# Optimization experiments

Measured on AMD Instinct MI355X. Metric: run time of the kernel, lower is better.

Reference implementation:

```python
import jax, jax.numpy as jnp
import numpy as np

B, L, E, H = 4, 1024, 1024, 16
D = E // H  # head_dim = 64
K = 3       # conv kernel size
PROB = 0.9  # Bernoulli keep probability


def setup_inputs() -> dict:
    key = jax.random.key(0)
    ks = jax.random.split(key, 8)
    query = jax.random.normal(ks[0], (B, L, E), dtype=jnp.float32)
    keys = jax.random.normal(ks[1], (B, L, E), dtype=jnp.float32)
    values = jax.random.normal(ks[2], (B, L, E), dtype=jnp.float32)
    padding_mask = jax.random.randint(ks[3], (B, L), 0, 2, dtype=jnp.int32)
    causal_mask = jax.random.randint(ks[4], (B, L), 0, 2, dtype=jnp.int32)
    bern_mask = jax.random.bernoulli(ks[5], PROB, (B, H, L)).astype(jnp.int32)
    # learned params: grouped conv (one in/out channel per head) and value linear
    conv_w = jax.random.normal(ks[6], (H, 1, K, K), dtype=jnp.float32) * 0.1
    conv_b = jnp.zeros((H,), dtype=jnp.float32)
    Wv = jax.random.normal(ks[7], (D, D), dtype=jnp.float32) / np.sqrt(D)
    return {"query": query, "keys": keys, "values": values,
            "padding_mask": padding_mask, "causal_mask": causal_mask,
            "bern_mask": bern_mask, "conv_w": conv_w, "conv_b": conv_b, "Wv": Wv}


def _split_heads(x):  # [b, l, (h d)] -> [b, h, l, d]
    b, l, _ = x.shape
    return x.reshape(b, l, H, D).transpose(0, 2, 1, 3)


def reference(query, keys, values, padding_mask, causal_mask, bern_mask, conv_w, conv_b, Wv):
    # queries: grouped conv2d over [b, h=channels, l, d], shape-preserving
    q = _split_heads(query)
    q = jax.lax.conv_general_dilated(
        q, conv_w, window_strides=(1, 1), padding=((1, 1), (1, 1)),
        dimension_numbers=("NCHW", "OIHW", "NCHW"), feature_group_count=H)
    q = q + conv_b[None, :, None, None]
    # keys: Bernoulli-masked fill with -inf, softmax over the SEQ dim (dim=-2)
    k = _split_heads(keys)
    k = jnp.where(bern_mask[..., None].astype(bool), k, -jnp.inf)
    k = jax.nn.softmax(k, axis=-2)
    # values: per-head linear (torch Linear: x @ W^T)
    v = jnp.einsum("bhld,ed->bhle", _split_heads(values), Wv)
    # attention
    energy = jnp.einsum("bhqd,bhkd->bhqk", q, k)
    mask = (padding_mask.astype(bool) & causal_mask.astype(bool))  # [b, k]
    energy = jnp.where(mask[:, None, None, :], jnp.float32(-1e20), energy)
    attn = jax.nn.softmax(energy / jnp.sqrt(jnp.float32(E)), axis=-1)
    out = jnp.einsum("bhqk,bhkd->bhqd", attn, v)
    return out.transpose(0, 2, 1, 3).reshape(query.shape[0], query.shape[1], E)
```

## Files before the change

### kernel.cpp

```cpp
#include <hip/hip_runtime.h>
#include <hip/hip_bf16.h>
#include <math.h>

#define BB 4
#define LL 1024
#define EE 1024
#define HH 16
#define DD 64
#define NCH 8
#define CHROWS 128
#define K2C 0.04508422002777998f
#define BIASC 7.2134752044448f

typedef __attribute__((ext_vector_type(8))) short short8;
typedef __attribute__((ext_vector_type(4))) float f32x4;
typedef __attribute__((ext_vector_type(4))) int int4v;

static __device__ __forceinline__ unsigned short bfbits(float x) {
    __hip_bfloat16 h = __float2bfloat16(x);
    return *(unsigned short*)&h;
}

#define CVTPK(dst, lo_, hi_) \
    asm("v_cvt_pk_bf16_f32 %0, %1, %2" : "=v"(dst) : "v"(lo_), "v"(hi_))

__global__ __launch_bounds__(256) void prep_kernel(
    const float* __restrict__ query,
    const float* __restrict__ conv_w,
    const float* __restrict__ conv_b,
    const float* __restrict__ values,
    const float* __restrict__ Wv,
    const float* __restrict__ keys,
    const int* __restrict__ bern,
    const int* __restrict__ pad,
    const int* __restrict__ cau,
    __hip_bfloat16* __restrict__ qcb,
    __hip_bfloat16* __restrict__ vt,
    float* __restrict__ pmax,
    float* __restrict__ psum,
    float* __restrict__ mbias) {
    __shared__ __align__(16) char SM[34048];
    int tid = threadIdx.x;
    int bid = blockIdx.x;

    if (bid < 4096) {
        int d = tid & 63;
        int lr = tid >> 6;
        int l0 = (bid & (LL / 4 - 1)) << 2;
        int bh = bid >> 8;
        int h = bh & (HH - 1);
        int b = bh >> 4;
        int l = l0 + lr;

        const float* w = conv_w + h * 9;
        float acc = conv_b[h];
        const float* qin = query + ((size_t)b * LL) * EE + h * DD;
        #pragma unroll
        for (int i = 0; i < 3; ++i) {
            int li = l + i - 1;
            if (li < 0 || li >= LL) continue;
            #pragma unroll
            for (int j = 0; j < 3; ++j) {
                int dj = d + j - 1;
                if (dj < 0 || dj >= DD) continue;
                acc += w[i * 3 + j] * qin[(size_t)li * EE + dj];
            }
        }
        qcb[((size_t)bh * LL + l) * DD + d] = __float2bfloat16(acc);
    } else if (bid < 5120) {
        float (*WvS)[65] = (float(*)[65])SM;
        float (*vs)[68]  = (float(*)[68])(SM + 16640);
        int tile = bid - 4096;
        int lt = tile & 15;
        int bh = tile >> 4;
        int h = bh & (HH - 1);
        int b = bh >> 4;
        int l0 = lt * 64;

        for (int idx = tid; idx < 64 * 64; idx += 256)
            WvS[idx >> 6][idx & 63] = Wv[idx];
        const float* vin = values + ((size_t)b * LL + l0) * EE + h * DD;
        for (int idx = tid; idx < 1024; idx += 256) {
            int r = idx >> 4;
            int c4 = (idx & 15) << 2;
            *(float4*)&vs[r][c4] = *(const float4*)&vin[(size_t)r * EE + c4];
        }
        __syncthreads();

        int d = tid & 63;
        int r0 = (tid >> 6) * 16;
        float acc[16];
        #pragma unroll
        for (int r = 0; r < 16; ++r) acc[r] = 0.f;
        for (int k = 0; k < 64; ++k) {
            float wv = WvS[d][k];
            #pragma unroll
            for (int r = 0; r < 16; ++r) acc[r] += vs[r0 + r][k] * wv;
        }
        union { unsigned short us[16]; uint2 u2[4]; } pk;
        #pragma unroll
        for (int r = 0; r < 16; ++r) pk.us[r] = bfbits(acc[r]);
        int C32 = (r0 >> 5) << 5;
        int h4 = (r0 >> 4) & 1;
        __hip_bfloat16* vo = vt + ((size_t)bh * DD + d) * LL + l0 + C32 + 4 * h4;
        #pragma unroll
        for (int g2 = 0; g2 < 4; ++g2)
            *(uint2*)&vo[8 * g2] = pk.u2[g2];
    } else {
        float (*sm)[64] = (float(*)[64])SM;
        float (*ss)[64] = (float(*)[64])(SM + 1024);
        int blk = bid - 5120;
        int d = tid & 63;
        int seg = tid >> 6;
        int ch = blk & (NCH - 1);
        int bh = blk >> 3;
        int h = bh & (HH - 1);
        int b = bh >> 4;
        int r0 = ch * CHROWS + seg * 32;

        if (h == 0 && tid < CHROWS) {
            int l = ch * CHROWS + tid;
            int msk = (pad[b * LL + l] != 0) & (cau[b * LL + l] != 0);
            mbias[b * LL + l] = msk ? (-1e20f * K2C - BIASC) : -BIASC;
        }

        const float* kin = keys + ((size_t)b * LL + r0) * EE + h * DD + d;
        const int* bm = bern + (size_t)bh * LL + r0;

        float v[32];
        #pragma unroll
        for (int i = 0; i < 32; ++i) v[i] = kin[(size_t)i * EE];
        float m = -INFINITY;
        #pragma unroll
        for (int i = 0; i < 32; ++i)
            if (bm[i]) m = fmaxf(m, v[i]);
        float s = 0.f;
        #pragma unroll
        for (int i = 0; i < 32; ++i)
            if (bm[i]) s += __expf(v[i] - m);

        sm[seg][d] = m;
        ss[seg][d] = s;
        __syncthreads();
        if (seg == 0) {
            float M = sm[0][d];
            #pragma unroll
            for (int t = 1; t < 4; ++t) M = fmaxf(M, sm[t][d]);
            float S = 0.f;
            if (M > -INFINITY) {
                #pragma unroll
                for (int t = 0; t < 4; ++t)
                    if (sm[t][d] > -INFINITY) S += ss[t][d] * __expf(sm[t][d] - M);
            }
            pmax[(size_t)blk * 64 + d] = M;
            psum[(size_t)blk * 64 + d] = S;
        }
    }
}

__global__ __launch_bounds__(256) void ksm_final_kernel(
    const float* __restrict__ keys,
    const int* __restrict__ bern,
    const float* __restrict__ pmax,
    const float* __restrict__ psum,
    __hip_bfloat16* __restrict__ ksb) {
    int tid = threadIdx.x;
    int d = tid & 63;
    int seg = tid >> 6;
    int blk = blockIdx.x;
    int ch = blk & (NCH - 1);
    int bh = blk >> 3;
    int h = bh & (HH - 1);
    int b = bh >> 4;
    int r0 = ch * CHROWS + seg * 32;

    const float* pm = pmax + (size_t)bh * NCH * 64;
    const float* ps = psum + (size_t)bh * NCH * 64;
    float M = -INFINITY;
    #pragma unroll
    for (int c = 0; c < NCH; ++c) M = fmaxf(M, pm[c * 64 + d]);
    float S = 0.f;
    #pragma unroll
    for (int c = 0; c < NCH; ++c) {
        float mi = pm[c * 64 + d];
        if (mi > -INFINITY) S += ps[c * 64 + d] * __expf(mi - M);
    }
    float inv = 1.f / S;

    const float* kin = keys + ((size_t)b * LL + r0) * EE + h * DD + d;
    const int* bm = bern + (size_t)bh * LL + r0;
    __hip_bfloat16* kout = ksb + ((size_t)bh * LL + r0) * DD + d;
    #pragma unroll
    for (int i = 0; i < 32; ++i) {
        float val = bm[i] ? __expf(kin[(size_t)i * EE] - M) * inv : 0.f;
        kout[(size_t)i * DD] = __float2bfloat16(val);
    }
}

__global__ __launch_bounds__(256) void attn_mfma_kernel(
    const __hip_bfloat16* __restrict__ qcb,
    const __hip_bfloat16* __restrict__ ksb,
    const __hip_bfloat16* __restrict__ vtb,
    const float* __restrict__ mbias,
    float* __restrict__ out) {
    __shared__ __align__(16) short KsS[2][4096];
    __shared__ __align__(16) short VtS[2][4096];
    __shared__ __align__(16) float mskS[1024];

    int tid = threadIdx.x;
    int lane = tid & 63;
    int w = tid >> 6;
    int q15 = lane & 15;
    int g = (lane >> 4) & 3;

    int bid = blockIdx.x;
    int swz = (bid & 7) * 128 + (bid >> 3);
    int bh = swz >> 4;
    int qb = swz & 15;
    int b = bh >> 4;
    int h = bh & 15;
    int q0w = qb * 64 + w * 16;

    int srow = tid >> 3;
    int sch = tid & 7;
    int ssw = (sch ^ (srow & 7)) << 3;
    const short* kg = (const short*)ksb + (size_t)bh * LL * DD + (size_t)srow * DD + ssw;
    const short* vg = (const short*)vtb + (size_t)bh * DD * LL + (size_t)srow * LL + ssw;

    short8 Qf0, Qf1;
    {
        const short* qrow = (const short*)qcb + ((size_t)bh * LL + q0w + q15) * DD + 8 * g;
        Qf0 = *(const short8*)(qrow);
        Qf1 = *(const short8*)(qrow + 32);
    }

    __builtin_amdgcn_global_load_lds(
        (const __attribute__((address_space(1))) void*)(mbias + b * LL + tid * 4),
        (__attribute__((address_space(3))) void*)&mskS[w * 256], 16, 0, 0);
    #pragma unroll
    for (int it = 0; it < 2; ++it) {
        __builtin_amdgcn_global_load_lds(
            (const __attribute__((address_space(1))) void*)(kg + (size_t)(it * 32) * DD),
            (__attribute__((address_space(3))) void*)&KsS[0][(it * 4 + w) * 512], 16, 0, 0);
        __builtin_amdgcn_global_load_lds(
            (const __attribute__((address_space(1))) void*)(vg + (size_t)it * 32 * LL),
            (__attribute__((address_space(3))) void*)&VtS[0][(it * 4 + w) * 512], 16, 0, 0);
    }

    f32x4 O[4];
    #pragma unroll
    for (int u = 0; u < 4; ++u) O[u] = (f32x4){0.f, 0.f, 0.f, 0.f};
    float lsum = 0.f;

    for (int kt = 0; kt < 16; ++kt) {
        __syncthreads();

        if (kt < 15) {
            int nb = (kt + 1) & 1;
            int k0n = (kt + 1) * 64;
            #pragma unroll
            for (int it = 0; it < 2; ++it) {
                __builtin_amdgcn_global_load_lds(
                    (const __attribute__((address_space(1))) void*)(kg + (size_t)(k0n + it * 32) * DD),
                    (__attribute__((address_space(3))) void*)&KsS[nb][(it * 4 + w) * 512], 16, 0, 0);
                __builtin_amdgcn_global_load_lds(
                    (const __attribute__((address_space(1))) void*)(vg + k0n + (size_t)it * 32 * LL),
                    (__attribute__((address_space(3))) void*)&VtS[nb][(it * 4 + w) * 512], 16, 0, 0);
            }
        }

        int cb = kt & 1;
        int k0 = kt * 64;
        const short* Kb = KsS[cb];
        const short* Vb = VtS[cb];
        int sw = q15 & 7;
        int off0 = (g ^ sw) << 3;
        int off1 = ((g + 4) ^ sw) << 3;

        f32x4 S[4];
        __builtin_amdgcn_s_setprio(1);
        #pragma unroll
        for (int t = 0; t < 4; ++t) {
            short8 kf0 = *(const short8*)&Kb[(16 * t + q15) * 64 + off0];
            short8 kf1 = *(const short8*)&Kb[(16 * t + q15) * 64 + off1];
            f32x4 z = (f32x4){0.f, 0.f, 0.f, 0.f};
            z = __builtin_amdgcn_mfma_f32_16x16x32_bf16(kf0, Qf0, z, 0, 0, 0);
            S[t] = __builtin_amdgcn_mfma_f32_16x16x32_bf16(kf1, Qf1, z, 0, 0, 0);
        }
        __builtin_amdgcn_s_setprio(0);

        float4 mb[4];
        #pragma unroll
        for (int t = 0; t < 4; ++t)
            mb[t] = *(const float4*)&mskS[k0 + 16 * t + 4 * g];
        float pv[4][4];
        #pragma unroll
        for (int t = 0; t < 4; ++t)
            #pragma unroll
            for (int r = 0; r < 4; ++r)
                pv[t][r] = exp2f(__builtin_fmaf(S[t][r], K2C, mb[t][r]));

        float s0 = (pv[0][0] + pv[0][1]) + (pv[0][2] + pv[0][3]);
        float s1 = (pv[1][0] + pv[1][1]) + (pv[1][2] + pv[1][3]);
        float s2 = (pv[2][0] + pv[2][1]) + (pv[2][2] + pv[2][3]);
        float s3 = (pv[3][0] + pv[3][1]) + (pv[3][2] + pv[3][3]);
        lsum += (s0 + s1) + (s2 + s3);

        int4v pa0, pa1;
        {
            int d0, d1, d2, d3;
            CVTPK(d0, pv[0][0], pv[0][1]);
            CVTPK(d1, pv[0][2], pv[0][3]);
            CVTPK(d2, pv[1][0], pv[1][1]);
            CVTPK(d3, pv[1][2], pv[1][3]);
            pa0 = (int4v){d0, d1, d2, d3};
            CVTPK(d0, pv[2][0], pv[2][1]);
            CVTPK(d1, pv[2][2], pv[2][3]);
            CVTPK(d2, pv[3][0], pv[3][1]);
            CVTPK(d3, pv[3][2], pv[3][3]);
            pa1 = (int4v){d0, d1, d2, d3};
        }
        union PW { int4v i4; short8 s8; } pw0, pw1;
        pw0.i4 = pa0;
        pw1.i4 = pa1;

        __builtin_amdgcn_s_setprio(1);
        #pragma unroll
        for (int u = 0; u < 4; ++u) {
            short8 vf0 = *(const short8*)&Vb[(16 * u + q15) * 64 + off0];
            short8 vf1 = *(const short8*)&Vb[(16 * u + q15) * 64 + off1];
            O[u] = __builtin_amdgcn_mfma_f32_16x16x32_bf16(vf0, pw0.s8, O[u], 0, 0, 0);
            O[u] = __builtin_amdgcn_mfma_f32_16x16x32_bf16(vf1, pw1.s8, O[u], 0, 0, 0);
        }
        __builtin_amdgcn_s_setprio(0);
    }

    lsum += __shfl_xor(lsum, 16, 64);
    lsum += __shfl_xor(lsum, 32, 64);
    float invl = 1.f / lsum;

    float* gout = out + ((size_t)b * LL + q0w + q15) * EE + h * DD + 4 * g;
    #pragma unroll
    for (int u = 0; u < 4; ++u) {
        float4 vv = { O[u][0] * invl, O[u][1] * invl, O[u][2] * invl, O[u][3] * invl };
        *(float4*)&gout[16 * u] = vv;
    }
}

extern "C" void kernel_launch(void* const* d_in, const int* in_sizes, int n_in,
                              void* d_out, int out_size, void* d_ws, size_t ws_size,
                              hipStream_t stream) {
    const float* query = (const float*)d_in[0];
    const float* keys  = (const float*)d_in[1];
    const float* values = (const float*)d_in[2];
    const int* pad  = (const int*)d_in[3];
    const int* cau  = (const int*)d_in[4];
    const int* bern = (const int*)d_in[5];
    const float* conv_w = (const float*)d_in[6];
    const float* conv_b = (const float*)d_in[7];
    const float* Wv = (const float*)d_in[8];
    float* outp = (float*)d_out;

    const size_t per = (size_t)BB * HH * LL * DD;
    __hip_bfloat16* qcb = (__hip_bfloat16*)d_ws;
    __hip_bfloat16* ksb = qcb + per;
    __hip_bfloat16* vtb = ksb + per;
    float* pmax = (float*)(vtb + per);
    float* psum = pmax + (size_t)BB * HH * NCH * 64;
    float* mbias = psum + (size_t)BB * HH * NCH * 64;

    prep_kernel<<<5632, 256, 0, stream>>>(query, conv_w, conv_b, values, Wv,
                                          keys, bern, pad, cau,
                                          qcb, vtb, pmax, psum, mbias);
    ksm_final_kernel<<<BB * HH * NCH, 256, 0, stream>>>(keys, bern, pmax, psum, ksb);
    attn_mfma_kernel<<<BB * HH * 16, 256, 0, stream>>>(qcb, ksb, vtb, mbias, outp);
}
```

Before: 76.86 us.

## Fold key mask into V and compute softmax denominator via extra MFMA row

Masked keys now have their V rows zeroed in the prep kernel. A mask-indicator row plus zero padding is appended to the transposed V (80 rows), so the attention kernel gets the softmax denominator from an extra MFMA tile instead of per-element mask bias loads and scalar lsum adds. The 1/sqrt(E)·log2e scale is pre-multiplied into the bf16 conv query, removing the per-element FMA before exp2. This trades two extra MFMAs and extra V LDS traffic per tile for fewer VALU ops. It changes the numerics: there is no max/bias subtraction, and a query row whose keys are all masked would divide by zero.

```diff
diff --git a/kernel.cpp b/kernel.cpp
--- a/kernel.cpp
+++ b/kernel.cpp
@@ -7,10 +7,10 @@
 #define EE 1024
 #define HH 16
 #define DD 64
+#define VROWS 80
 #define NCH 8
 #define CHROWS 128
 #define K2C 0.04508422002777998f
-#define BIASC 7.2134752044448f
 
 typedef __attribute__((ext_vector_type(8))) short short8;
 typedef __attribute__((ext_vector_type(4))) float f32x4;
@@ -37,9 +37,8 @@
     __hip_bfloat16* __restrict__ qcb,
     __hip_bfloat16* __restrict__ vt,
     float* __restrict__ pmax,
-    float* __restrict__ psum,
-    float* __restrict__ mbias) {
-    __shared__ __align__(16) char SM[34048];
+    float* __restrict__ psum) {
+    __shared__ __align__(16) char SM[34304];
     int tid = threadIdx.x;
     int bid = blockIdx.x;
 
@@ -66,10 +65,11 @@
                 acc += w[i * 3 + j] * qin[(size_t)li * EE + dj];
             }
         }
-        qcb[((size_t)bh * LL + l) * DD + d] = __float2bfloat16(acc);
+        qcb[((size_t)bh * LL + l) * DD + d] = __float2bfloat16(acc * K2C);
     } else if (bid < 5120) {
         float (*WvS)[65] = (float(*)[65])SM;
         float (*vs)[68]  = (float(*)[68])(SM + 16640);
+        float* mS = (float*)(SM + 34048);
         int tile = bid - 4096;
         int lt = tile & 15;
         int bh = tile >> 4;
@@ -77,6 +77,10 @@
         int b = bh >> 4;
         int l0 = lt * 64;
 
+        if (tid < 64) {
+            int l = l0 + tid;
+            mS[tid] = ((pad[b * LL + l] != 0) & (cau[b * LL + l] != 0)) ? 0.f : 1.f;
+        }
         for (int idx = tid; idx < 64 * 64; idx += 256)
             WvS[idx >> 6][idx & 63] = Wv[idx];
         const float* vin = values + ((size_t)b * LL + l0) * EE + h * DD;
@@ -97,15 +101,28 @@
             #pragma unroll
             for (int r = 0; r < 16; ++r) acc[r] += vs[r0 + r][k] * wv;
         }
+        #pragma unroll
+        for (int r = 0; r < 16; ++r) acc[r] *= mS[r0 + r];
         union { unsigned short us[16]; uint2 u2[4]; } pk;
         #pragma unroll
         for (int r = 0; r < 16; ++r) pk.us[r] = bfbits(acc[r]);
-        int C32 = (r0 >> 5) << 5;
-        int h4 = (r0 >> 4) & 1;
-        __hip_bfloat16* vo = vt + ((size_t)bh * DD + d) * LL + l0 + C32 + 4 * h4;
+        int a = tid >> 6;
+        int C32 = (a >> 1) << 5;
+        int h4 = a & 1;
+        __hip_bfloat16* vo = vt + ((size_t)bh * VROWS + d) * LL + l0 + C32 + 4 * h4;
         #pragma unroll
         for (int g2 = 0; g2 < 4; ++g2)
             *(uint2*)&vo[8 * g2] = pk.u2[g2];
+
+        if (tid < 64) {
+            int aa = tid >> 4, g2 = (tid >> 2) & 3, m = tid & 3;
+            int dst = l0 + 32 * (aa >> 1) + 4 * (aa & 1) + 8 * g2 + m;
+            vt[((size_t)bh * VROWS + 64) * LL + dst] = __float2bfloat16(mS[tid]);
+        }
+        for (int idx = tid; idx < 15 * 64; idx += 256) {
+            int rr = idx >> 6, l = idx & 63;
+            vt[((size_t)bh * VROWS + 65 + rr) * LL + l0 + l] = __float2bfloat16(0.f);
+        }
     } else {
         float (*sm)[64] = (float(*)[64])SM;
         float (*ss)[64] = (float(*)[64])(SM + 1024);
@@ -117,12 +134,6 @@
         int h = bh & (HH - 1);
         int b = bh >> 4;
         int r0 = ch * CHROWS + seg * 32;
-
-        if (h == 0 && tid < CHROWS) {
-            int l = ch * CHROWS + tid;
-            int msk = (pad[b * LL + l] != 0) & (cau[b * LL + l] != 0);
-            mbias[b * LL + l] = msk ? (-1e20f * K2C - BIASC) : -BIASC;
-        }
 
         const float* kin = keys + ((size_t)b * LL + r0) * EE + h * DD + d;
         const int* bm = bern + (size_t)bh * LL + r0;
@@ -201,11 +212,9 @@
     const __hip_bfloat16* __restrict__ qcb,
     const __hip_bfloat16* __restrict__ ksb,
     const __hip_bfloat16* __restrict__ vtb,
-    const float* __restrict__ mbias,
     float* __restrict__ out) {
     __shared__ __align__(16) short KsS[2][4096];
-    __shared__ __align__(16) short VtS[2][4096];
-    __shared__ __align__(16) float mskS[1024];
+    __shared__ __align__(16) short VtS[2][5120];
 
     int tid = threadIdx.x;
     int lane = tid & 63;
@@ -225,7 +234,8 @@
     int sch = tid & 7;
     int ssw = (sch ^ (srow & 7)) << 3;
     const short* kg = (const short*)ksb + (size_t)bh * LL * DD + (size_t)srow * DD + ssw;
-    const short* vg = (const short*)vtb + (size_t)bh * DD * LL + (size_t)srow * LL + ssw;
+    const short* vg = (const short*)vtb + (size_t)bh * VROWS * LL + (size_t)srow * LL + ssw;
+    const short* vgx = (const short*)vtb + (size_t)bh * VROWS * LL + (size_t)(64 + srow) * LL + ssw;
 
     short8 Qf0, Qf1;
     {
@@ -234,9 +244,6 @@
         Qf1 = *(const short8*)(qrow + 32);
     }
 
-    __builtin_amdgcn_global_load_lds(
-        (const __attribute__((address_space(1))) void*)(mbias + b * LL + tid * 4),
-        (__attribute__((address_space(3))) void*)&mskS[w * 256], 16, 0, 0);
     #pragma unroll
     for (int it = 0; it < 2; ++it) {
         __builtin_amdgcn_global_load_lds(
@@ -246,11 +253,16 @@
             (const __attribute__((address_space(1))) void*)(vg + (size_t)it * 32 * LL),
             (__attribute__((address_space(3))) void*)&VtS[0][(it * 4 + w) * 512], 16, 0, 0);
     }
-
-    f32x4 O[4];
+    if (w < 2) {
+        __builtin_amdgcn_global_load_lds(
+            (const __attribute__((address_space(1))) void*)(vgx),
+            (__attribute__((address_space(3))) void*)&VtS[0][4096 + w * 512], 16, 0, 0);
+    }
+
+    f32x4 O[4], O5;
     #pragma unroll
     for (int u = 0; u < 4; ++u) O[u] = (f32x4){0.f, 0.f, 0.f, 0.f};
-    float lsum = 0.f;
+    O5 = (f32x4){0.f, 0.f, 0.f, 0.f};
 
     for (int kt = 0; kt < 16; ++kt) {
         __syncthreads();
@@ -267,10 +279,14 @@
                     (const __attribute__((address_space(1))) void*)(vg + k0n + (size_t)it * 32 * LL),
                     (__attribute__((address_space(3))) void*)&VtS[nb][(it * 4 + w) * 512], 16, 0, 0);
             }
+            if (w < 2) {
+                __builtin_amdgcn_global_load_lds(
+                    (const __attribute__((address_space(1))) void*)(vgx + k0n),
+                    (__attribute__((address_space(3))) void*)&VtS[nb][4096 + w * 512], 16, 0, 0);
+            }
         }
 
         int cb = kt & 1;
-        int k0 = kt * 64;
         const short* Kb = KsS[cb];
         const short* Vb = VtS[cb];
         int sw = q15 & 7;
@@ -289,22 +305,19 @@
         }
         __builtin_amdgcn_s_setprio(0);
 
-        float4 mb[4];
+        short8 vfa[5], vfb[5];
+        #pragma unroll
+        for (int u = 0; u < 5; ++u) {
+            vfa[u] = *(const short8*)&Vb[(16 * u + q15) * 64 + off0];
+            vfb[u] = *(const short8*)&Vb[(16 * u + q15) * 64 + off1];
+        }
+
+        float pv[4][4];
         #pragma unroll
         for (int t = 0; t < 4; ++t)
-            mb[t] = *(const float4*)&mskS[k0 + 16 * t + 4 * g];
-        float pv[4][4];
-        #pragma unroll
-        for (int t = 0; t < 4; ++t)
             #pragma unroll
             for (int r = 0; r < 4; ++r)
-                pv[t][r] = exp2f(__builtin_fmaf(S[t][r], K2C, mb[t][r]));
-
-        float s0 = (pv[0][0] + pv[0][1]) + (pv[0][2] + pv[0][3]);
-        float s1 = (pv[1][0] + pv[1][1]) + (pv[1][2] + pv[1][3]);
-        float s2 = (pv[2][0] + pv[2][1]) + (pv[2][2] + pv[2][3]);
-        float s3 = (pv[3][0] + pv[3][1]) + (pv[3][2] + pv[3][3]);
-        lsum += (s0 + s1) + (s2 + s3);
+                pv[t][r] = exp2f(S[t][r]);
 
         int4v pa0, pa1;
         {
@@ -327,17 +340,16 @@
         __builtin_amdgcn_s_setprio(1);
         #pragma unroll
         for (int u = 0; u < 4; ++u) {
-            short8 vf0 = *(const short8*)&Vb[(16 * u + q15) * 64 + off0];
-            short8 vf1 = *(const short8*)&Vb[(16 * u + q15) * 64 + off1];
-            O[u] = __builtin_amdgcn_mfma_f32_16x16x32_bf16(vf0, pw0.s8, O[u], 0, 0, 0);
-            O[u] = __builtin_amdgcn_mfma_f32_16x16x32_bf16(vf1, pw1.s8, O[u], 0, 0, 0);
-        }
+            O[u] = __builtin_amdgcn_mfma_f32_16x16x32_bf16(vfa[u], pw0.s8, O[u], 0, 0, 0);
+            O[u] = __builtin_amdgcn_mfma_f32_16x16x32_bf16(vfb[u], pw1.s8, O[u], 0, 0, 0);
+        }
+        O5 = __builtin_amdgcn_mfma_f32_16x16x32_bf16(vfa[4], pw0.s8, O5, 0, 0, 0);
+        O5 = __builtin_amdgcn_mfma_f32_16x16x32_bf16(vfb[4], pw1.s8, O5, 0, 0, 0);
         __builtin_amdgcn_s_setprio(0);
     }
 
-    lsum += __shfl_xor(lsum, 16, 64);
-    lsum += __shfl_xor(lsum, 32, 64);
-    float invl = 1.f / lsum;
+    float ls = __shfl(O5[0], q15, 64);
+    float invl = 1.f / ls;
 
     float* gout = out + ((size_t)b * LL + q0w + q15) * EE + h * DD + 4 * g;
     #pragma unroll
@@ -362,16 +374,16 @@
     float* outp = (float*)d_out;
 
     const size_t per = (size_t)BB * HH * LL * DD;
+    const size_t vper = (size_t)BB * HH * VROWS * LL;
     __hip_bfloat16* qcb = (__hip_bfloat16*)d_ws;
     __hip_bfloat16* ksb = qcb + per;
     __hip_bfloat16* vtb = ksb + per;
-    float* pmax = (float*)(vtb + per);
+    float* pmax = (float*)(vtb + vper);
     float* psum = pmax + (size_t)BB * HH * NCH * 64;
-    float* mbias = psum + (size_t)BB * HH * NCH * 64;
 
     prep_kernel<<<5632, 256, 0, stream>>>(query, conv_w, conv_b, values, Wv,
                                           keys, bern, pad, cau,
-                                          qcb, vtb, pmax, psum, mbias);
+                                          qcb, vtb, pmax, psum);
     ksm_final_kernel<<<BB * HH * NCH, 256, 0, stream>>>(keys, bern, pmax, psum, ksb);
-    attn_mfma_kernel<<<BB * HH * 16, 256, 0, stream>>>(qcb, ksb, vtb, mbias, outp);
-}
+    attn_mfma_kernel<<<BB * HH * 16, 256, 0, stream>>>(qcb, ksb, vtb, outp);
+}
```

Result: faster. 74.67 us (-2.9%).
